# Performance work log

Measured on AMD Instinct MI355X. Metric: run time of the kernel, lower is better.

## Reference

```python
import jax, jax.numpy as jnp
import numpy as np

CACHE_LEN = 1024
EPS = 1e-5

def layer_norm(x, g, b):
    m = jnp.mean(x, axis=-1, keepdims=True)
    var = jnp.mean(jnp.square(x - m), axis=-1, keepdims=True)
    return (x - m) * jax.lax.rsqrt(var + EPS) * g + b

def setup_inputs() -> dict:
    key = jax.random.key(0)
    ks = jax.random.split(key, 16)
    B, Lq, Lk, D_IN, D_OUT = 4, 4096, 5119, 512, 512
    s = 1.0 / np.sqrt(D_IN)
    return {
        "q": jax.random.normal(ks[0], (B, Lq, D_IN), jnp.float32),
        "k": jax.random.normal(ks[1], (B, Lk, D_IN), jnp.float32),
        "v": jax.random.normal(ks[2], (B, Lk, D_IN), jnp.float32),
        "gq": jnp.ones((D_IN,), jnp.float32),
        "bq": jnp.zeros((D_IN,), jnp.float32),
        "gk": jnp.ones((D_IN,), jnp.float32),
        "bk": jnp.zeros((D_IN,), jnp.float32),
        "gv": jnp.ones((D_IN,), jnp.float32),
        "bv": jnp.zeros((D_IN,), jnp.float32),
        "Wq": jax.random.uniform(ks[3], (D_IN, D_OUT), jnp.float32, -s, s),
        "bwq": jax.random.uniform(ks[4], (D_OUT,), jnp.float32, -s, s),
        "Wk": jax.random.uniform(ks[5], (D_IN, D_OUT), jnp.float32, -s, s),
        "bwk": jax.random.uniform(ks[6], (D_OUT,), jnp.float32, -s, s),
        "Wv": jax.random.uniform(ks[7], (D_IN, D_OUT), jnp.float32, -s, s),
        "bwv": jax.random.uniform(ks[8], (D_OUT,), jnp.float32, -s, s),
    }

def reference(q, k, v, gq, bq, gk, bk, gv, bv, Wq, bwq, Wk, bwk, Wv, bwv):
    B, Lq, _ = q.shape
    Lk = k.shape[1]
    qp = layer_norm(q, gq, bq) @ Wq + bwq            # [B,Lq,Do]
    kp = layer_norm(k, gk, bk) @ Wk + bwk            # [B,Lk,Do]
    vp = layer_norm(v, gv, bv) @ Wv + bwv            # [B,Lk,Do]
    kv = jax.nn.relu(kp) * vp                         # [B,Lk,Do]
    # integrate3 skew-pad builds a banded ones mask: query row i attends to
    # kv columns [sup+i, sup+i+cache_len-1]. Equivalent sliding-window sum
    # computed via prefix sums (O(Lk*d) instead of O(Lq*Lk*d)).
    sup = Lk - Lq - CACHE_LEN + 1
    cs = jnp.cumsum(kv, axis=1)
    cs = jnp.concatenate([jnp.zeros_like(cs[:, :1]), cs], axis=1)  # [B,Lk+1,Do]
    starts = sup + jnp.arange(Lq)
    weighted = cs[:, starts + CACHE_LEN] - cs[:, starts]            # [B,Lq,Do]
    return jax.nn.relu(qp) * weighted
```

## Files before the change

kernel.cpp:

```cpp
#include <hip/hip_runtime.h>

#define B     4
#define LQ    4096
#define LK    5119
#define LKP   5120
#define D     512
#define CACHE 1024
#define MQ    (B * LQ)
#define MKP   (B * LKP)
#define NCH   160
#define TI    32

typedef float  f32x4  __attribute__((ext_vector_type(4)));
typedef __bf16 bf16x2 __attribute__((ext_vector_type(2)));
typedef __bf16 bf16x8 __attribute__((ext_vector_type(8)));

__device__ __forceinline__ void async16(void* lds, const void* g)
{
    __builtin_amdgcn_global_load_lds(
        (__attribute__((address_space(1))) void*)(g),
        (__attribute__((address_space(3))) void*)(lds),
        16, 0, 0);
}

__global__ __launch_bounds__(256) void prep_kernel(
    const float* __restrict__ q, const float* __restrict__ k,
    const float* __restrict__ v,
    const float* __restrict__ gq, const float* __restrict__ bq,
    const float* __restrict__ gk, const float* __restrict__ bk,
    const float* __restrict__ gv, const float* __restrict__ bv,
    const float* __restrict__ Wq, const float* __restrict__ Wk,
    const float* __restrict__ Wv,
    __bf16* __restrict__ qn, __bf16* __restrict__ kn, __bf16* __restrict__ vn,
    __bf16* __restrict__ wtq, __bf16* __restrict__ wtk, __bf16* __restrict__ wtv)
{
    const int z = blockIdx.y;

    if (z == 3) {
        const int idx = blockIdx.x;
        if (idx >= 384) return;
        const int zz  = idx >> 7;
        const int rem = idx & 127;
        const float* W = (zz == 0) ? Wq : (zz == 1) ? Wk : Wv;
        __bf16*     Wt = (zz == 0) ? wtq : (zz == 1) ? wtk : wtv;
        const int n  = (rem & 1) * 256 + threadIdx.x;
        const int k0 = (rem >> 1) * 8;
        bf16x8 o;
#pragma unroll
        for (int j = 0; j < 8; ++j)
            o[j] = (__bf16)W[(long)(k0 + j) * D + n];
        *reinterpret_cast<bf16x8*>(Wt + (long)n * D + k0) = o;
        return;
    }

    const float *x, *g, *bb; __bf16* o;
    if (z == 0)      { x = q; g = gq; bb = bq; o = qn; }
    else if (z == 1) { x = k; g = gk; bb = bk; o = kn; }
    else             { x = v; g = gv; bb = bv; o = vn; }

    const int rp = blockIdx.x * 8 + (threadIdx.x >> 5);
    long rin;
    if (z == 0) {
        if (rp >= MQ) return;
        rin = rp;
    } else {
        const int bch = rp / LKP;
        const int i   = rp - bch * LKP;
        if (i == LK) return;
        rin = (long)bch * LK + i;
    }

    const int c0 = (threadIdx.x & 31) * 16;
    const float* xr = x + rin * D + c0;

    float4 a[4];
#pragma unroll
    for (int j = 0; j < 4; ++j)
        a[j] = *reinterpret_cast<const float4*>(xr + j * 4);

    float s = 0.f, ss = 0.f;
#pragma unroll
    for (int j = 0; j < 4; ++j) {
        s  += a[j].x + a[j].y + a[j].z + a[j].w;
        ss += a[j].x*a[j].x + a[j].y*a[j].y + a[j].z*a[j].z + a[j].w*a[j].w;
    }
#pragma unroll
    for (int m = 1; m <= 16; m <<= 1) {
        s  += __shfl_xor(s,  m, 64);
        ss += __shfl_xor(ss, m, 64);
    }
    const float mean = s * (1.f / (float)D);
    const float var  = ss * (1.f / (float)D) - mean * mean;
    const float rs   = rsqrtf(var + 1e-5f);

    bf16x8 o0, o1;
#pragma unroll
    for (int j = 0; j < 4; ++j) {
        const float4 gv4 = *reinterpret_cast<const float4*>(g  + c0 + j * 4);
        const float4 bv4 = *reinterpret_cast<const float4*>(bb + c0 + j * 4);
        const float y0 = (a[j].x - mean) * rs * gv4.x + bv4.x;
        const float y1 = (a[j].y - mean) * rs * gv4.y + bv4.y;
        const float y2 = (a[j].z - mean) * rs * gv4.z + bv4.z;
        const float y3 = (a[j].w - mean) * rs * gv4.w + bv4.w;
        if (j < 2) {
            o0[j*4+0] = (__bf16)y0; o0[j*4+1] = (__bf16)y1;
            o0[j*4+2] = (__bf16)y2; o0[j*4+3] = (__bf16)y3;
        } else {
            o1[(j-2)*4+0] = (__bf16)y0; o1[(j-2)*4+1] = (__bf16)y1;
            o1[(j-2)*4+2] = (__bf16)y2; o1[(j-2)*4+3] = (__bf16)y3;
        }
    }
    __bf16* orow = o + (long)rp * D + c0;
    *reinterpret_cast<bf16x8*>(orow)     = o0;
    *reinterpret_cast<bf16x8*>(orow + 8) = o1;
}

__global__ __launch_bounds__(256, 2) void gemm_fused_kernel(
    const __bf16* __restrict__ qn, const __bf16* __restrict__ kn,
    const __bf16* __restrict__ vn,
    const __bf16* __restrict__ wtq, const __bf16* __restrict__ wtk,
    const __bf16* __restrict__ wtv,
    const float* __restrict__ bwq, const float* __restrict__ bwk,
    const float* __restrict__ bwv,
    __bf16* __restrict__ qpb, __bf16* __restrict__ kvb,
    float* __restrict__ Csum)
{
    __shared__ __attribute__((aligned(16))) __bf16 smem[32768];

    const int bid  = blockIdx.x;
    const int tid  = threadIdx.x;
    const int lane = tid & 63;
    const int wave = tid >> 6;
    const int quad = lane >> 4;
    const int l16  = lane & 15;
    const int wm   = wave >> 1;
    const int wn   = wave & 1;
    const int lrow = lane >> 3;
    const int lcs  = ((lane & 7) ^ lrow) * 8;

    if (bid < 512) {
        __bf16* As = smem;
        __bf16* Bs = smem + 8192;

        f32x4 acc[4][4];
#pragma unroll
        for (int i = 0; i < 4; ++i)
#pragma unroll
            for (int j = 0; j < 4; ++j)
                acc[i][j] = (f32x4){0.f, 0.f, 0.f, 0.f};

        const long arow0 = (long)(bid & 127) * 128;
        const long brow0 = (long)(bid >> 7) * 128;

        for (int k0 = 0; k0 < D; k0 += 64) {
#pragma unroll
            for (int j = 0; j < 4; ++j) {
                const int r0  = (j * 4 + wave) * 8;
                const int row = r0 + lrow;
                async16(&As[r0 * 64], &qn [(arow0 + row) * D + k0 + lcs]);
                async16(&Bs[r0 * 64], &wtq[(brow0 + row) * D + k0 + lcs]);
            }
            __syncthreads();

            bf16x8 af[4][2], bf[4][2];
#pragma unroll
            for (int tm = 0; tm < 4; ++tm) {
                const int m = wm * 64 + tm * 16 + l16;
#pragma unroll
                for (int kh = 0; kh < 2; ++kh)
                    af[tm][kh] = *reinterpret_cast<const bf16x8*>(
                        &As[m * 64 + (((kh * 4 + quad) ^ (m & 7)) * 8)]);
            }
#pragma unroll
            for (int tn = 0; tn < 4; ++tn) {
                const int n = wn * 64 + tn * 16 + l16;
#pragma unroll
                for (int kh = 0; kh < 2; ++kh)
                    bf[tn][kh] = *reinterpret_cast<const bf16x8*>(
                        &Bs[n * 64 + (((kh * 4 + quad) ^ (n & 7)) * 8)]);
            }
#pragma unroll
            for (int kh = 0; kh < 2; ++kh)
#pragma unroll
                for (int tm = 0; tm < 4; ++tm)
#pragma unroll
                    for (int tn = 0; tn < 4; ++tn)
                        acc[tm][tn] = __builtin_amdgcn_mfma_f32_16x16x32_bf16(
                            af[tm][kh], bf[tn][kh], acc[tm][tn], 0, 0, 0);
            __syncthreads();
        }

#pragma unroll
        for (int tm = 0; tm < 4; ++tm) {
            const long row0 = arow0 + wm * 64 + tm * 16 + quad * 4;
#pragma unroll
            for (int tn = 0; tn < 4; ++tn) {
                const int col = (int)brow0 + wn * 64 + tn * 16 + l16;
                const float bv = bwq[col];
#pragma unroll
                for (int r = 0; r < 4; ++r)
                    qpb[(row0 + r) * D + col] =
                        (__bf16)fmaxf(acc[tm][tn][r] + bv, 0.f);
            }
        }
    } else {
        __bf16* Ks  = smem;
        __bf16* Vs  = smem + 8192;
        __bf16* WKs = smem + 16384;
        __bf16* WVs = smem + 24576;

        const int bid2  = bid - 512;
        const int ntile = bid2 / 160;
        const int mtile = bid2 - ntile * 160;

        f32x4 acck[4][4], accv[4][4];
#pragma unroll
        for (int i = 0; i < 4; ++i)
#pragma unroll
            for (int j = 0; j < 4; ++j) {
                acck[i][j] = (f32x4){0.f, 0.f, 0.f, 0.f};
                accv[i][j] = (f32x4){0.f, 0.f, 0.f, 0.f};
            }

        const long arow0 = (long)mtile * 128;
        const long brow0 = (long)ntile * 128;

        for (int k0 = 0; k0 < D; k0 += 64) {
#pragma unroll
            for (int j = 0; j < 4; ++j) {
                const int r0  = (j * 4 + wave) * 8;
                const int row = r0 + lrow;
                async16(&Ks [r0 * 64], &kn [(arow0 + row) * D + k0 + lcs]);
                async16(&Vs [r0 * 64], &vn [(arow0 + row) * D + k0 + lcs]);
                async16(&WKs[r0 * 64], &wtk[(brow0 + row) * D + k0 + lcs]);
                async16(&WVs[r0 * 64], &wtv[(brow0 + row) * D + k0 + lcs]);
            }
            __syncthreads();

            bf16x8 fa[4][2], fb[4][2];
#pragma unroll
            for (int tm = 0; tm < 4; ++tm) {
                const int m = wm * 64 + tm * 16 + l16;
#pragma unroll
                for (int kh = 0; kh < 2; ++kh)
                    fa[tm][kh] = *reinterpret_cast<const bf16x8*>(
                        &Ks[m * 64 + (((kh * 4 + quad) ^ (m & 7)) * 8)]);
            }
#pragma unroll
            for (int tn = 0; tn < 4; ++tn) {
                const int n = wn * 64 + tn * 16 + l16;
#pragma unroll
                for (int kh = 0; kh < 2; ++kh)
                    fb[tn][kh] = *reinterpret_cast<const bf16x8*>(
                        &WKs[n * 64 + (((kh * 4 + quad) ^ (n & 7)) * 8)]);
            }
#pragma unroll
            for (int kh = 0; kh < 2; ++kh)
#pragma unroll
                for (int tm = 0; tm < 4; ++tm)
#pragma unroll
                    for (int tn = 0; tn < 4; ++tn)
                        acck[tm][tn] = __builtin_amdgcn_mfma_f32_16x16x32_bf16(
                            fa[tm][kh], fb[tn][kh], acck[tm][tn], 0, 0, 0);
#pragma unroll
            for (int tm = 0; tm < 4; ++tm) {
                const int m = wm * 64 + tm * 16 + l16;
#pragma unroll
                for (int kh = 0; kh < 2; ++kh)
                    fa[tm][kh] = *reinterpret_cast<const bf16x8*>(
                        &Vs[m * 64 + (((kh * 4 + quad) ^ (m & 7)) * 8)]);
            }
#pragma unroll
            for (int tn = 0; tn < 4; ++tn) {
                const int n = wn * 64 + tn * 16 + l16;
#pragma unroll
                for (int kh = 0; kh < 2; ++kh)
                    fb[tn][kh] = *reinterpret_cast<const bf16x8*>(
                        &WVs[n * 64 + (((kh * 4 + quad) ^ (n & 7)) * 8)]);
            }
#pragma unroll
            for (int kh = 0; kh < 2; ++kh)
#pragma unroll
                for (int tm = 0; tm < 4; ++tm)
#pragma unroll
                    for (int tn = 0; tn < 4; ++tn)
                        accv[tm][tn] = __builtin_amdgcn_mfma_f32_16x16x32_bf16(
                            fa[tm][kh], fb[tn][kh], accv[tm][tn], 0, 0, 0);
            __syncthreads();
        }

        float part[4][2];
#pragma unroll
        for (int tn = 0; tn < 4; ++tn) { part[tn][0] = 0.f; part[tn][1] = 0.f; }
#pragma unroll
        for (int tm = 0; tm < 4; ++tm) {
            const long row0 = arow0 + wm * 64 + tm * 16 + quad * 4;
#pragma unroll
            for (int tn = 0; tn < 4; ++tn) {
                const int col = (int)brow0 + wn * 64 + tn * 16 + l16;
                const float bkc = bwk[col];
                const float bvc = bwv[col];
#pragma unroll
                for (int r = 0; r < 4; ++r) {
                    const float kp = fmaxf(acck[tm][tn][r] + bkc, 0.f);
                    const float vp = accv[tm][tn][r] + bvc;
                    const __bf16 kb = (__bf16)(kp * vp);
                    kvb[(row0 + r) * D + col] = kb;
                    part[tn][tm >> 1] += (float)kb;
                }
            }
        }
#pragma unroll
        for (int tn = 0; tn < 4; ++tn)
#pragma unroll
            for (int th = 0; th < 2; ++th) {
                float vv = part[tn][th];
                vv += __shfl_xor(vv, 16, 64);
                vv += __shfl_xor(vv, 32, 64);
                if (quad == 0) {
                    const int fc = ((int)(arow0 >> 5)) + wm * 2 + th;
                    const int bb = fc / NCH;
                    const int cc = fc - bb * NCH;
                    const int col = (int)brow0 + wn * 64 + tn * 16 + l16;
                    Csum[((long)bb * NCH + cc) * D + col] = vv;
                }
            }
    }
}

__global__ __launch_bounds__(256) void window_kernel(
    const __bf16* __restrict__ kv, const float* __restrict__ Csum,
    const __bf16* __restrict__ qpb, float* __restrict__ out)
{
    const int iq   = blockIdx.x;
    const int b    = blockIdx.y;
    const int i0   = iq * TI;
    const int col2 = threadIdx.x * 2;

    const float* cs = Csum + (long)b * NCH * D + col2;
    float s0 = 0.f, s1 = 0.f;
#pragma unroll
    for (int c = 0; c < 32; ++c) {
        const float2 cv = *reinterpret_cast<const float2*>(cs + (long)(iq + c) * D);
        s0 += cv.x; s1 += cv.y;
    }

    const __bf16* kvb = kv  + (long)b * LKP * D + col2;
    const __bf16* qb  = qpb + (long)b * LQ  * D + col2;
    float*        ob  = out + (long)b * LQ  * D + col2;

#pragma unroll 8
    for (int i = i0; i < i0 + TI; ++i) {
        const bf16x2 qv = *reinterpret_cast<const bf16x2*>(qb + (long)i * D);
        *reinterpret_cast<float2*>(ob + (long)i * D) =
            make_float2((float)qv[0] * s0, (float)qv[1] * s1);
        const bf16x2 lead  = *reinterpret_cast<const bf16x2*>(kvb + (long)(i + CACHE) * D);
        const bf16x2 trail = *reinterpret_cast<const bf16x2*>(kvb + (long)i * D);
        s0 += (float)lead[0] - (float)trail[0];
        s1 += (float)lead[1] - (float)trail[1];
    }
}

extern "C" void kernel_launch(void* const* d_in, const int* in_sizes, int n_in,
                              void* d_out, int out_size, void* d_ws, size_t ws_size,
                              hipStream_t stream)
{
    const float* q   = (const float*)d_in[0];
    const float* k   = (const float*)d_in[1];
    const float* v   = (const float*)d_in[2];
    const float* gq  = (const float*)d_in[3];
    const float* bq  = (const float*)d_in[4];
    const float* gk  = (const float*)d_in[5];
    const float* bk  = (const float*)d_in[6];
    const float* gv  = (const float*)d_in[7];
    const float* bv  = (const float*)d_in[8];
    const float* Wq  = (const float*)d_in[9];
    const float* bwq = (const float*)d_in[10];
    const float* Wk  = (const float*)d_in[11];
    const float* bwk = (const float*)d_in[12];
    const float* Wv  = (const float*)d_in[13];
    const float* bwv = (const float*)d_in[14];
    float* out = (float*)d_out;

    char* ws = (char*)d_ws;
    __bf16* qn   = (__bf16*)ws;
    __bf16* kn   = qn  + (long)MQ  * D;
    __bf16* vn   = kn  + (long)MKP * D;
    __bf16* qpb  = vn  + (long)MKP * D;
    __bf16* kvb  = qpb + (long)MQ  * D;
    __bf16* wtq  = kvb + (long)MKP * D;
    __bf16* wtk  = wtq + (long)D * D;
    __bf16* wtv  = wtk + (long)D * D;
    float*  Csum = (float*)(wtv + (long)D * D);

    prep_kernel<<<dim3(2560, 4), 256, 0, stream>>>(
        q, k, v, gq, bq, gk, bk, gv, bv, Wq, Wk, Wv,
        qn, kn, vn, wtq, wtk, wtv);

    gemm_fused_kernel<<<512 + 640, 256, 0, stream>>>(
        qn, kn, vn, wtq, wtk, wtv, bwq, bwk, bwv, qpb, kvb, Csum);

    window_kernel<<<dim3(LQ / TI, B), 256, 0, stream>>>(kvb, Csum, qpb, out);
}
```

Before: 233.1 us.

## Reorder GEMM blocks so heavy KV tiles go first and prefetch next K-tile

New measurement: 232.2 us. About the same (-0.4%).

```diff
diff --git a/kernel.cpp b/kernel.cpp
--- a/kernel.cpp
+++ b/kernel.cpp
@@ -138,80 +138,14 @@
     const int lrow = lane >> 3;
     const int lcs  = ((lane & 7) ^ lrow) * 8;
 
-    if (bid < 512) {
-        __bf16* As = smem;
-        __bf16* Bs = smem + 8192;
-
-        f32x4 acc[4][4];
-#pragma unroll
-        for (int i = 0; i < 4; ++i)
-#pragma unroll
-            for (int j = 0; j < 4; ++j)
-                acc[i][j] = (f32x4){0.f, 0.f, 0.f, 0.f};
-
-        const long arow0 = (long)(bid & 127) * 128;
-        const long brow0 = (long)(bid >> 7) * 128;
-
-        for (int k0 = 0; k0 < D; k0 += 64) {
-#pragma unroll
-            for (int j = 0; j < 4; ++j) {
-                const int r0  = (j * 4 + wave) * 8;
-                const int row = r0 + lrow;
-                async16(&As[r0 * 64], &qn [(arow0 + row) * D + k0 + lcs]);
-                async16(&Bs[r0 * 64], &wtq[(brow0 + row) * D + k0 + lcs]);
-            }
-            __syncthreads();
-
-            bf16x8 af[4][2], bf[4][2];
-#pragma unroll
-            for (int tm = 0; tm < 4; ++tm) {
-                const int m = wm * 64 + tm * 16 + l16;
-#pragma unroll
-                for (int kh = 0; kh < 2; ++kh)
-                    af[tm][kh] = *reinterpret_cast<const bf16x8*>(
-                        &As[m * 64 + (((kh * 4 + quad) ^ (m & 7)) * 8)]);
-            }
-#pragma unroll
-            for (int tn = 0; tn < 4; ++tn) {
-                const int n = wn * 64 + tn * 16 + l16;
-#pragma unroll
-                for (int kh = 0; kh < 2; ++kh)
-                    bf[tn][kh] = *reinterpret_cast<const bf16x8*>(
-                        &Bs[n * 64 + (((kh * 4 + quad) ^ (n & 7)) * 8)]);
-            }
-#pragma unroll
-            for (int kh = 0; kh < 2; ++kh)
-#pragma unroll
-                for (int tm = 0; tm < 4; ++tm)
-#pragma unroll
-                    for (int tn = 0; tn < 4; ++tn)
-                        acc[tm][tn] = __builtin_amdgcn_mfma_f32_16x16x32_bf16(
-                            af[tm][kh], bf[tn][kh], acc[tm][tn], 0, 0, 0);
-            __syncthreads();
-        }
-
-#pragma unroll
-        for (int tm = 0; tm < 4; ++tm) {
-            const long row0 = arow0 + wm * 64 + tm * 16 + quad * 4;
-#pragma unroll
-            for (int tn = 0; tn < 4; ++tn) {
-                const int col = (int)brow0 + wn * 64 + tn * 16 + l16;
-                const float bv = bwq[col];
-#pragma unroll
-                for (int r = 0; r < 4; ++r)
-                    qpb[(row0 + r) * D + col] =
-                        (__bf16)fmaxf(acc[tm][tn][r] + bv, 0.f);
-            }
-        }
-    } else {
+    if (bid < 640) {
         __bf16* Ks  = smem;
         __bf16* Vs  = smem + 8192;
         __bf16* WKs = smem + 16384;
         __bf16* WVs = smem + 24576;
 
-        const int bid2  = bid - 512;
-        const int ntile = bid2 / 160;
-        const int mtile = bid2 - ntile * 160;
+        const int ntile = bid / 160;
+        const int mtile = bid - ntile * 160;
 
         f32x4 acck[4][4], accv[4][4];
 #pragma unroll
@@ -225,16 +159,20 @@
         const long arow0 = (long)mtile * 128;
         const long brow0 = (long)ntile * 128;
 
-        for (int k0 = 0; k0 < D; k0 += 64) {
+        auto stage_kv = [&](int kk) {
 #pragma unroll
             for (int j = 0; j < 4; ++j) {
                 const int r0  = (j * 4 + wave) * 8;
                 const int row = r0 + lrow;
-                async16(&Ks [r0 * 64], &kn [(arow0 + row) * D + k0 + lcs]);
-                async16(&Vs [r0 * 64], &vn [(arow0 + row) * D + k0 + lcs]);
-                async16(&WKs[r0 * 64], &wtk[(brow0 + row) * D + k0 + lcs]);
-                async16(&WVs[r0 * 64], &wtv[(brow0 + row) * D + k0 + lcs]);
-            }
+                async16(&Ks [r0 * 64], &kn [(arow0 + row) * D + kk + lcs]);
+                async16(&Vs [r0 * 64], &vn [(arow0 + row) * D + kk + lcs]);
+                async16(&WKs[r0 * 64], &wtk[(brow0 + row) * D + kk + lcs]);
+                async16(&WVs[r0 * 64], &wtv[(brow0 + row) * D + kk + lcs]);
+            }
+        };
+
+        stage_kv(0);
+        for (int kt = 0; kt < 8; ++kt) {
             __syncthreads();
 
             bf16x8 fa[4][2], fb[4][2];
@@ -278,6 +216,8 @@
                     fb[tn][kh] = *reinterpret_cast<const bf16x8*>(
                         &WVs[n * 64 + (((kh * 4 + quad) ^ (n & 7)) * 8)]);
             }
+            __syncthreads();
+            if (kt < 7) stage_kv((kt + 1) * 64);
 #pragma unroll
             for (int kh = 0; kh < 2; ++kh)
 #pragma unroll
@@ -286,7 +226,6 @@
                     for (int tn = 0; tn < 4; ++tn)
                         accv[tm][tn] = __builtin_amdgcn_mfma_f32_16x16x32_bf16(
                             fa[tm][kh], fb[tn][kh], accv[tm][tn], 0, 0, 0);
-            __syncthreads();
         }
 
         float part[4][2];
@@ -325,6 +264,78 @@
                     Csum[((long)bb * NCH + cc) * D + col] = vv;
                 }
             }
+    } else {
+        __bf16* As = smem;
+        __bf16* Bs = smem + 8192;
+
+        const int bidq = bid - 640;
+
+        f32x4 acc[4][4];
+#pragma unroll
+        for (int i = 0; i < 4; ++i)
+#pragma unroll
+            for (int j = 0; j < 4; ++j)
+                acc[i][j] = (f32x4){0.f, 0.f, 0.f, 0.f};
+
+        const long arow0 = (long)(bidq & 127) * 128;
+        const long brow0 = (long)(bidq >> 7) * 128;
+
+        auto stage_q = [&](int kk) {
+#pragma unroll
+            for (int j = 0; j < 4; ++j) {
+                const int r0  = (j * 4 + wave) * 8;
+                const int row = r0 + lrow;
+                async16(&As[r0 * 64], &qn [(arow0 + row) * D + kk + lcs]);
+                async16(&Bs[r0 * 64], &wtq[(brow0 + row) * D + kk + lcs]);
+            }
+        };
+
+        stage_q(0);
+        for (int kt = 0; kt < 8; ++kt) {
+            __syncthreads();
+
+            bf16x8 af[4][2], bf[4][2];
+#pragma unroll
+            for (int tm = 0; tm < 4; ++tm) {
+                const int m = wm * 64 + tm * 16 + l16;
+#pragma unroll
+                for (int kh = 0; kh < 2; ++kh)
+                    af[tm][kh] = *reinterpret_cast<const bf16x8*>(
+                        &As[m * 64 + (((kh * 4 + quad) ^ (m & 7)) * 8)]);
+            }
+#pragma unroll
+            for (int tn = 0; tn < 4; ++tn) {
+                const int n = wn * 64 + tn * 16 + l16;
+#pragma unroll
+                for (int kh = 0; kh < 2; ++kh)
+                    bf[tn][kh] = *reinterpret_cast<const bf16x8*>(
+                        &Bs[n * 64 + (((kh * 4 + quad) ^ (n & 7)) * 8)]);
+            }
+            __syncthreads();
+            if (kt < 7) stage_q((kt + 1) * 64);
+#pragma unroll
+            for (int kh = 0; kh < 2; ++kh)
+#pragma unroll
+                for (int tm = 0; tm < 4; ++tm)
+#pragma unroll
+                    for (int tn = 0; tn < 4; ++tn)
+                        acc[tm][tn] = __builtin_amdgcn_mfma_f32_16x16x32_bf16(
+                            af[tm][kh], bf[tn][kh], acc[tm][tn], 0, 0, 0);
+        }
+
+#pragma unroll
+        for (int tm = 0; tm < 4; ++tm) {
+            const long row0 = arow0 + wm * 64 + tm * 16 + quad * 4;
+#pragma unroll
+            for (int tn = 0; tn < 4; ++tn) {
+                const int col = (int)brow0 + wn * 64 + tn * 16 + l16;
+                const float bv = bwq[col];
+#pragma unroll
+                for (int r = 0; r < 4; ++r)
+                    qpb[(row0 + r) * D + col] =
+                        (__bf16)fmaxf(acc[tm][tn][r] + bv, 0.f);
+            }
+        }
     }
 }
 
@@ -397,7 +408,7 @@
         q, k, v, gq, bq, gk, bk, gv, bv, Wq, Wk, Wv,
         qn, kn, vn, wtq, wtk, wtv);
 
-    gemm_fused_kernel<<<512 + 640, 256, 0, stream>>>(
+    gemm_fused_kernel<<<640 + 512, 256, 0, stream>>>(
         qn, kn, vn, wtq, wtk, wtv, bwq, bwk, bwv, qpb, kvb, Csum);
 
     window_kernel<<<dim3(LQ / TI, B), 256, 0, stream>>>(kvb, Csum, qpb, out);
```
